# Optimization experiments

Measured on AMD Instinct MI355X. Metric: run time of the kernel, lower is better.

## Reference

```python
import jax, jax.numpy as jnp
import numpy as np
from functools import partial

B, H, W = 2, 480, 480
C, HALF = 32, 16
L, WN, PAD = 4, 20, 20

def gelu(x):
    return jax.nn.gelu(x, approximate=False)

def setup_inputs() -> dict:
    key = jax.random.key(0)
    ks = jax.random.split(key, 24)
    scale = 1.0 / (C * C)
    d = {}
    d["input_data"] = jax.random.normal(ks[0], (B, H, W, 1), jnp.float32)
    d["src_data"] = jax.random.normal(ks[1], (B, H, W, 3), jnp.float32)
    # input lifting MLP: sizes [5, 16, 32]
    d["in_w1"] = jax.random.normal(ks[2], (5, HALF), jnp.float32) * 0.1
    d["in_b1"] = jnp.zeros((HALF,), jnp.float32)
    d["in_w2"] = jax.random.normal(ks[3], (HALF, C), jnp.float32) * 0.1
    d["in_b2"] = jnp.zeros((C,), jnp.float32)
    # eps lifting MLP: sizes [3, 16, 32]
    d["eps_w1"] = jax.random.normal(ks[4], (3, HALF), jnp.float32) * 0.1
    d["eps_b1"] = jnp.zeros((HALF,), jnp.float32)
    d["eps_w2"] = jax.random.normal(ks[5], (HALF, C), jnp.float32) * 0.1
    d["eps_b2"] = jnp.zeros((C,), jnp.float32)
    # Fourier layer params, stacked over L layers
    d["fw1"] = jax.random.uniform(ks[6], (L, C, C, WN, WN, 2), jnp.float32) * scale
    d["fw2"] = jax.random.uniform(ks[7], (L, C, C, WN, WN, 2), jnp.float32) * scale
    d["conv_w"] = jax.random.normal(ks[8], (L, C, C), jnp.float32) * 0.05
    d["conv_b"] = jnp.zeros((L, C), jnp.float32)
    # projection MLP: sizes [32, 16, 2]
    d["proj_w1"] = jax.random.normal(ks[9], (C, HALF), jnp.float32) * 0.1
    d["proj_b1"] = jnp.zeros((HALF,), jnp.float32)
    d["proj_w2"] = jax.random.normal(ks[10], (HALF, 2), jnp.float32) * 0.1
    d["proj_b2"] = jnp.zeros((2,), jnp.float32)
    # mask conv 3x3, 1->1 channel
    d["mask_w"] = jax.random.normal(ks[11], (1, 1, 3, 3), jnp.float32) * 0.1
    d["mask_b"] = jnp.zeros((1,), jnp.float32)
    return d

def _grid(b, h, w):
    gx = jnp.broadcast_to(jnp.linspace(0.0, 1.0, h, dtype=jnp.float32)[None, :, None, None], (b, h, w, 1))
    gy = jnp.broadcast_to(jnp.linspace(0.0, 1.0, w, dtype=jnp.float32)[None, None, :, None], (b, h, w, 1))
    return jnp.concatenate([gx, gy], axis=-1)

def _mlp(x, w1, b1, w2, b2):
    # FCLayer(gelu) then FCLayer(linear)
    return gelu(x @ w1 + b1) @ w2 + b2

def _fourier_conv(x, x_eps, w1, w2):
    # x, x_eps: [B, C, Hp, Wp]
    hp, wp = x.shape[-2], x.shape[-1]
    xf = jnp.fft.rfft2(x * x_eps)                       # [B,C,Hp,Wp//2+1] complex
    xr = jnp.stack([xf.real, xf.imag], axis=-1)         # [B,C,Hp,Wp//2+1,2]
    lo = jnp.einsum('bixyz,ioxyz->boxyz', xr[:, :, :WN, :WN, :], w1)
    hi = jnp.einsum('bixyz,ioxyz->boxyz', xr[:, :, -WN:, :WN, :], w2)
    out = jnp.zeros((x.shape[0], w1.shape[1], hp, wp // 2 + 1, 2), jnp.float32)
    out = out.at[:, :, :WN, :WN, :].set(lo)
    out = out.at[:, :, -WN:, :WN, :].set(hi)
    return jnp.fft.irfft2(out[..., 0] + 1j * out[..., 1], s=(hp, wp))

def _forward(input_data, src_data, in_w1, in_b1, in_w2, in_b2,
             eps_w1, eps_b1, eps_w2, eps_b2, fw1, fw2, conv_w, conv_b,
             proj_w1, proj_b1, proj_w2, proj_b2, mask_w, mask_b):
    b, h, w = input_data.shape[0], input_data.shape[1], input_data.shape[2]
    grid = _grid(b, h, w)
    x_in = jnp.concatenate([src_data, grid], axis=-1)       # [B,H,W,5]
    x_eps = jnp.concatenate([input_data, grid], axis=-1)    # [B,H,W,3]
    field = src_data[..., 1:]                               # [B,H,W,2]

    a = _mlp(x_in, in_w1, in_b1, in_w2, in_b2)              # [B,H,W,C]
    a = jnp.transpose(a, (0, 3, 1, 2))                      # [B,C,H,W]
    a = jnp.pad(a, ((0, 0), (0, 0), (0, PAD), (0, PAD)))    # [B,C,H+P,W+P]
    e = _mlp(x_eps, eps_w1, eps_b1, eps_w2, eps_b2)
    e = jnp.transpose(e, (0, 3, 1, 2))
    e = jnp.pad(e, ((0, 0), (0, 0), (0, PAD), (0, PAD)))

    for l in range(L):
        x1 = _fourier_conv(a, e, fw1[l], fw2[l])
        x2 = jnp.einsum('bihw,oi->bohw', a, conv_w[l]) + conv_b[l][None, :, None, None]
        a = x1 + x2
        if l < L - 1:
            a = gelu(a)

    pred = a[..., :-PAD, :-PAD]                             # [B,C,H,W]
    pred = jnp.transpose(pred, (0, 2, 3, 1))                # [B,H,W,C]
    pred = _mlp(pred, proj_w1, proj_b1, proj_w2, proj_b2)   # [B,H,W,2]

    xm = jnp.transpose(input_data, (0, 3, 1, 2))            # [B,1,H,W]
    mask = jax.lax.conv_general_dilated(xm, mask_w, (1, 1), 'SAME',
                                        dimension_numbers=('NCHW', 'OIHW', 'NCHW'))
    mask = mask + mask_b[None, :, None, None]
    mask = jnp.transpose(mask, (0, 2, 3, 1))                # [B,H,W,1] -> broadcasts over 2
    return field * mask + pred

def reference(input_data, src_data, in_w1, in_b1, in_w2, in_b2,
              eps_w1, eps_b1, eps_w2, eps_b2, fw1, fw2, conv_w, conv_b,
              proj_w1, proj_b1, proj_w2, proj_b2, mask_w, mask_b):
    return _forward(input_data, src_data, in_w1, in_b1, in_w2, in_b2,
                    eps_w1, eps_b1, eps_w2, eps_b2, fw1, fw2, conv_w, conv_b,
                    proj_w1, proj_b1, proj_w2, proj_b2, mask_w, mask_b)
```

## Files before the change

kernel.cpp:

```cpp
#include <hip/hip_runtime.h>
#include <hip/hip_bf16.h>

#define BD 2
#define HD 480
#define WD 480
#define CD 32
#define HALFD 16
#define WND 20
#define NP 500
#define PLANE (HD*WD)
#define TWO_PI_OVER_NP 0.012566370614359172954f

typedef __attribute__((ext_vector_type(8))) short bf16x8;
typedef __attribute__((ext_vector_type(4))) float f32x4;

__device__ __forceinline__ float gelu_f(float x) {
    return 0.5f * x * (1.0f + erff(x * 0.70710678118654752f));
}
__device__ __forceinline__ float bfbits2f(short s) {
    unsigned u = ((unsigned)(unsigned short)s) << 16;
    return __uint_as_float(u);
}
__device__ __forceinline__ short bf16s(float v) {
    __hip_bfloat16 b = __float2bfloat16(v);
    return *reinterpret_cast<short*>(&b);
}
__device__ __forceinline__ unsigned pk2(float a, float b) {
    return (unsigned)(unsigned short)bf16s(a) | ((unsigned)(unsigned short)bf16s(b) << 16);
}
__device__ __forceinline__ unsigned mulpk(unsigned a, unsigned e) {
    return pk2(bfbits2f((short)(a & 0xffff)) * bfbits2f((short)(e & 0xffff)),
               bfbits2f((short)(a >> 16))    * bfbits2f((short)(e >> 16)));
}

__global__ void __launch_bounds__(512) k_aeF1(
    const float* src, const float* inp,
    const float* iw1, const float* ib1,
    const float* iw2, const float* ib2,
    const float* ew1, const float* eb1,
    const float* ew2, const float* eb2,
    const __hip_bfloat16* Twig,
    __hip_bfloat16* A, __hip_bfloat16* E, __hip_bfloat16* Y1)
{
    __shared__ float s_iw1[80], s_ib1[16];
    __shared__ float s_ew1[48], s_eb1[16];
    __shared__ __align__(16) __hip_bfloat16 s_hid[480 * 16];
    __shared__ __align__(16) __hip_bfloat16 sA[32 * 488];

    int tid = threadIdx.x;
    int lane = tid & 63, wv = tid >> 6;
    int c0 = lane & 15, kg = lane >> 4;
    int b = blockIdx.x / HD;
    int h = blockIdx.x % HD;

    if (tid < 80) s_iw1[tid] = iw1[tid];
    if (tid >= 96 && tid < 112) s_ib1[tid - 96] = ib1[tid - 96];
    if (tid >= 128 && tid < 176) s_ew1[tid - 128] = ew1[tid - 128];
    if (tid >= 192 && tid < 208) s_eb1[tid - 192] = eb1[tid - 192];

    bf16x8 bIn[2], bEps[2];
    float biasIn[2], biasEps[2];
    #pragma unroll
    for (int nt = 0; nt < 2; nt++) {
        int c = nt * 16 + c0;
        #pragma unroll
        for (int j = 0; j < 8; j++) {
            int k = kg * 8 + j;
            bIn[nt][j]  = (k < 16) ? bf16s(iw2[k * 32 + c]) : (short)0;
            bEps[nt][j] = (k < 16) ? bf16s(ew2[k * 32 + c]) : (short)0;
        }
        biasIn[nt]  = ib2[c];
        biasEps[nt] = eb2[c];
    }

    float s0 = 0.f, s1 = 0.f, s2 = 0.f, xi = 0.f;
    float gx = (float)h * (1.0f / 479.0f);
    float gy = (float)tid * (1.0f / 479.0f);
    size_t pbase = (size_t)b * PLANE + (size_t)h * WD;
    if (tid < WD) {
        s0 = src[(pbase + tid) * 3 + 0];
        s1 = src[(pbase + tid) * 3 + 1];
        s2 = src[(pbase + tid) * 3 + 2];
        xi = inp[pbase + tid];
    }
    __syncthreads();

    if (tid < WD) {
        unsigned pk[8];
        #pragma unroll
        for (int j = 0; j < 16; j += 2) {
            float v0 = s_ib1[j]     + s0 * s_iw1[j]     + s1 * s_iw1[16 + j]
                     + s2 * s_iw1[32 + j]     + gx * s_iw1[48 + j]     + gy * s_iw1[64 + j];
            float v1 = s_ib1[j + 1] + s0 * s_iw1[j + 1] + s1 * s_iw1[16 + j + 1]
                     + s2 * s_iw1[32 + j + 1] + gx * s_iw1[48 + j + 1] + gy * s_iw1[64 + j + 1];
            pk[j >> 1] = pk2(gelu_f(v0), gelu_f(v1));
        }
        uint4* d = reinterpret_cast<uint4*>(&s_hid[tid * 16]);
        d[0] = make_uint4(pk[0], pk[1], pk[2], pk[3]);
        d[1] = make_uint4(pk[4], pk[5], pk[6], pk[7]);
    }
    __syncthreads();

    for (int t = wv; t < 60; t += 8) {
        int tile = t >> 1, nt = t & 1;
        bf16x8 av = {0, 0, 0, 0, 0, 0, 0, 0};
        if (kg < 2)
            av = *reinterpret_cast<const bf16x8*>(&s_hid[(tile * 16 + c0) * 16 + kg * 8]);
        f32x4 acc = {0.f, 0.f, 0.f, 0.f};
        acc = __builtin_amdgcn_mfma_f32_16x16x32_bf16(av, bIn[nt], acc, 0, 0, 0);
        float bias = biasIn[nt];
        int ch = nt * 16 + c0;
        int px = tile * 16 + kg * 4;
        unsigned w0 = pk2(acc[0] + bias, acc[1] + bias);
        unsigned w1 = pk2(acc[2] + bias, acc[3] + bias);
        *reinterpret_cast<uint2*>(&sA[ch * 488 + px]) = make_uint2(w0, w1);
    }
    __syncthreads();

    {
        __hip_bfloat16* Adst = A + (size_t)b * CD * PLANE + (size_t)h * WD;
        for (int t = tid; t < 32 * 60; t += 512) {
            int row = t / 60, chunk = t % 60;
            uint4 v = *reinterpret_cast<const uint4*>(&sA[row * 488 + chunk * 8]);
            *reinterpret_cast<uint4*>(&Adst[(size_t)row * PLANE + chunk * 8]) = v;
        }
    }
    if (tid < WD) {
        unsigned pk[8];
        #pragma unroll
        for (int j = 0; j < 16; j += 2) {
            float v0 = s_eb1[j]     + xi * s_ew1[j]     + gx * s_ew1[16 + j]     + gy * s_ew1[32 + j];
            float v1 = s_eb1[j + 1] + xi * s_ew1[j + 1] + gx * s_ew1[16 + j + 1] + gy * s_ew1[32 + j + 1];
            pk[j >> 1] = pk2(gelu_f(v0), gelu_f(v1));
        }
        uint4* d = reinterpret_cast<uint4*>(&s_hid[tid * 16]);
        d[0] = make_uint4(pk[0], pk[1], pk[2], pk[3]);
        d[1] = make_uint4(pk[4], pk[5], pk[6], pk[7]);
    }
    __syncthreads();

    for (int t = wv; t < 60; t += 8) {
        int tile = t >> 1, nt = t & 1;
        bf16x8 av = {0, 0, 0, 0, 0, 0, 0, 0};
        if (kg < 2)
            av = *reinterpret_cast<const bf16x8*>(&s_hid[(tile * 16 + c0) * 16 + kg * 8]);
        f32x4 acc = {0.f, 0.f, 0.f, 0.f};
        acc = __builtin_amdgcn_mfma_f32_16x16x32_bf16(av, bEps[nt], acc, 0, 0, 0);
        float bias = biasEps[nt];
        int ch = nt * 16 + c0;
        int px = tile * 16 + kg * 4;
        float e0 = acc[0] + bias, e1 = acc[1] + bias;
        float e2 = acc[2] + bias, e3 = acc[3] + bias;
        *reinterpret_cast<uint2*>(&E[(size_t)(b * 32 + ch) * PLANE + (size_t)h * WD + px])
            = make_uint2(pk2(e0, e1), pk2(e2, e3));
        uint2 a8 = *reinterpret_cast<const uint2*>(&sA[ch * 488 + px]);
        float a0 = bfbits2f((short)(a8.x & 0xffff));
        float a1 = bfbits2f((short)(a8.x >> 16));
        float a2 = bfbits2f((short)(a8.y & 0xffff));
        float a3 = bfbits2f((short)(a8.y >> 16));
        *reinterpret_cast<uint2*>(&sA[ch * 488 + px])
            = make_uint2(pk2(a0 * e0, a1 * e1), pk2(a2 * e2, a3 * e3));
    }
    __syncthreads();

    if (wv < 6) {
        int mt = wv & 1, nt = wv >> 1;
        int c = mt * 16 + c0;
        const __hip_bfloat16* gbase = &sA[c * 488 + (kg << 3)];
        f32x4 a0 = {0.f, 0.f, 0.f, 0.f}, a1 = a0, a2 = a0;
        #pragma unroll
        for (int kt = 0; kt < 15; kt += 3) {
            bf16x8 g0 = *reinterpret_cast<const bf16x8*>(gbase + kt * 32);
            bf16x8 g1 = *reinterpret_cast<const bf16x8*>(gbase + (kt + 1) * 32);
            bf16x8 g2 = *reinterpret_cast<const bf16x8*>(gbase + (kt + 2) * 32);
            bf16x8 b0 = *reinterpret_cast<const bf16x8*>(Twig + (((kt * 3 + nt) << 9) + lane * 8));
            bf16x8 b1 = *reinterpret_cast<const bf16x8*>(Twig + ((((kt + 1) * 3 + nt) << 9) + lane * 8));
            bf16x8 b2 = *reinterpret_cast<const bf16x8*>(Twig + ((((kt + 2) * 3 + nt) << 9) + lane * 8));
            a0 = __builtin_amdgcn_mfma_f32_16x16x32_bf16(g0, b0, a0, 0, 0, 0);
            a1 = __builtin_amdgcn_mfma_f32_16x16x32_bf16(g1, b1, a1, 0, 0, 0);
            a2 = __builtin_amdgcn_mfma_f32_16x16x32_bf16(g2, b2, a2, 0, 0, 0);
        }
        f32x4 acc = a0 + a1 + a2;
        int n = nt * 16 + c0;
        if (n < 40) {
            int ky = n >> 1, part = n & 1;
            int crow = mt * 16 + (kg << 2);
            #pragma unroll
            for (int r = 0; r < 4; r++) {
                int cc = crow + r;
                Y1[((((size_t)(b * 32 + cc)) * WND + ky) * HD + h) * 2 + part] =
                    __float2bfloat16(acc[r]);
            }
        }
    }
}

__global__ void k_tables(__hip_bfloat16* T) {
    int e = blockIdx.x * 256 + threadIdx.x;
    if (e >= 435 * 512) return;
    int tile = e >> 9, r = e & 511;
    int lane = r >> 3, j = r & 7;
    float v = 0.0f;
    if (tile < 45) {
        int kt = tile / 3, nt = tile % 3;
        int k = kt * 32 + ((lane >> 4) << 3) + j;
        int n = nt * 16 + (lane & 15);
        if (n < 40) {
            int ky = n >> 1;
            int idx = (k * ky) % NP;
            float ang = (float)idx * TWO_PI_OVER_NP;
            v = (n & 1) ? -sinf(ang) : cosf(ang);
        }
    } else if (tile < 105) {
        int t2 = tile - 45;
        int nt = t2 >> 1, kt = t2 & 1;
        int kk = kt * 32 + ((lane >> 4) << 3) + j;
        int w = nt * 16 + (lane & 15);
        if (kk < 40) {
            int ky = kk >> 1;
            int idx = (ky * w) % NP;
            float ang = (float)idx * TWO_PI_OVER_NP;
            v = (kk & 1) ? -sinf(ang) : cosf(ang);
        }
    } else if (tile < 255) {
        int t2 = tile - 105;
        int kt = t2 / 5, nt = t2 % 5;
        int k = kt * 32 + ((lane >> 4) << 3) + j;
        int n = nt * 16 + (lane & 15);
        int hh = k >> 1, ri = k & 1;
        int kxi = n >> 1, part = n & 1;
        int kx = (kxi < 20) ? kxi : kxi + 460;
        int idx = (kx * hh) % NP;
        float ang = (float)idx * TWO_PI_OVER_NP;
        float c = cosf(ang), s = sinf(ang);
        v = (part == 0) ? (ri == 0 ? c : s) : (ri == 0 ? -s : c);
    } else {
        int t2 = tile - 255;
        int nt = t2 / 3, kt = t2 % 3;
        int k = kt * 32 + ((lane >> 4) << 3) + j;
        int n = nt * 16 + (lane & 15);
        if (k < 80) {
            int kxi = k >> 1, ri = k & 1;
            int hh = n >> 1, part = n & 1;
            int kx = (kxi < 20) ? kxi : kxi + 460;
            int idx = (kx * hh) % NP;
            float ang = (float)idx * TWO_PI_OVER_NP;
            float c = cosf(ang), s = sinf(ang);
            v = (part == 0) ? (ri == 0 ? c : -s) : (ri == 0 ? s : c);
        }
    }
    T[e] = __float2bfloat16(v);
}

__global__ void __launch_bounds__(64) k_F2m(
    const __hip_bfloat16* Y1, const __hip_bfloat16* Tf2, float* Y2)
{
    int lane = threadIdx.x;
    int task = blockIdx.x;
    int mt = task / 5, nt = task % 5;
    int row = mt * 16 + (lane & 15);
    int koff = (lane >> 4) << 3;
    const __hip_bfloat16* arow = Y1 + (size_t)row * 960 + koff;
    f32x4 a0 = {0.f, 0.f, 0.f, 0.f}, a1 = a0, a2 = a0;
    #pragma unroll
    for (int kt = 0; kt < 30; kt += 3) {
        bf16x8 v0 = *reinterpret_cast<const bf16x8*>(arow + kt * 32);
        bf16x8 v1 = *reinterpret_cast<const bf16x8*>(arow + (kt + 1) * 32);
        bf16x8 v2 = *reinterpret_cast<const bf16x8*>(arow + (kt + 2) * 32);
        bf16x8 b0 = *reinterpret_cast<const bf16x8*>(Tf2 + (((kt * 5 + nt) << 9) + lane * 8));
        bf16x8 b1 = *reinterpret_cast<const bf16x8*>(Tf2 + ((((kt + 1) * 5 + nt) << 9) + lane * 8));
        bf16x8 b2 = *reinterpret_cast<const bf16x8*>(Tf2 + ((((kt + 2) * 5 + nt) << 9) + lane * 8));
        a0 = __builtin_amdgcn_mfma_f32_16x16x32_bf16(v0, b0, a0, 0, 0, 0);
        a1 = __builtin_amdgcn_mfma_f32_16x16x32_bf16(v1, b1, a1, 0, 0, 0);
        a2 = __builtin_amdgcn_mfma_f32_16x16x32_bf16(v2, b2, a2, 0, 0, 0);
    }
    f32x4 acc = a0 + a1 + a2;
    int n = nt * 16 + (lane & 15);
    int mb = mt * 16 + ((lane >> 4) << 2);
    #pragma unroll
    for (int r = 0; r < 4; r++)
        Y2[(size_t)(mb + r) * 80 + n] = acc[r];
}

__global__ void __launch_bounds__(256) k_mix(
    const float* Y2, __hip_bfloat16* Zb,
    const float* fw1, const float* fw2, int l)
{
    int gid = blockIdx.x * 256 + threadIdx.x;
    int col = gid % 96;
    int row = gid / 96;
    if (col >= 80) { Zb[gid] = __float2bfloat16(0.0f); return; }
    int ky = row % 20;
    int oc = (row / 20) % 32;
    int b = row / 640;
    int z = col & 1;
    int kxi = col >> 1;
    const float* wp;
    int x;
    if (kxi < 20) { wp = fw1; x = kxi; } else { wp = fw2; x = kxi - 20; }
    size_t wbase = ((((size_t)(l * 32) * 32 + oc) * 20 + x) * 20 + ky) * 2 + z;
    const float* y2 = Y2 + ((size_t)b * 32 * 20 + ky) * 80 + kxi * 2 + z;
    float acc = 0.f;
    for (int i = 0; i < 32; i++) {
        float yv = y2[(size_t)i * 1600];
        float wv = wp[wbase + (size_t)i * 25600];
        acc += yv * wv;
    }
    Zb[gid] = __float2bfloat16(acc);
}

__global__ void __launch_bounds__(256) k_I1m(
    const __hip_bfloat16* Zb, const __hip_bfloat16* Ti1, __hip_bfloat16* U)
{
    int wv = threadIdx.x >> 6, lane = threadIdx.x & 63;
    int task = blockIdx.x * 4 + wv;
    int mt = task / 60, nt = task % 60;
    int row = mt * 16 + (lane & 15);
    int koff = (lane >> 4) << 3;
    const __hip_bfloat16* arow = Zb + (size_t)row * 96 + koff;
    f32x4 a0 = {0.f, 0.f, 0.f, 0.f}, a1 = a0, a2 = a0;
    {
        bf16x8 v0 = *reinterpret_cast<const bf16x8*>(arow);
        bf16x8 v1 = *reinterpret_cast<const bf16x8*>(arow + 32);
        bf16x8 v2 = *reinterpret_cast<const bf16x8*>(arow + 64);
        bf16x8 b0 = *reinterpret_cast<const bf16x8*>(Ti1 + (((nt * 3 + 0) << 9) + lane * 8));
        bf16x8 b1 = *reinterpret_cast<const bf16x8*>(Ti1 + (((nt * 3 + 1) << 9) + lane * 8));
        bf16x8 b2 = *reinterpret_cast<const bf16x8*>(Ti1 + (((nt * 3 + 2) << 9) + lane * 8));
        a0 = __builtin_amdgcn_mfma_f32_16x16x32_bf16(v0, b0, a0, 0, 0, 0);
        a1 = __builtin_amdgcn_mfma_f32_16x16x32_bf16(v1, b1, a1, 0, 0, 0);
        a2 = __builtin_amdgcn_mfma_f32_16x16x32_bf16(v2, b2, a2, 0, 0, 0);
    }
    f32x4 acc = a0 + a1 + a2;
    int n = nt * 16 + (lane & 15);
    int mb = mt * 16 + ((lane >> 4) << 2);
    #pragma unroll
    for (int r = 0; r < 4; r++)
        U[(size_t)(mb + r) * 960 + n] = __float2bfloat16(acc[r]);
}

__global__ void __launch_bounds__(512) k_I2F1(
    const __hip_bfloat16* U, __hip_bfloat16* A,
    const __hip_bfloat16* E,
    const float* convw, const float* convb,
    const __hip_bfloat16* TinvF, const __hip_bfloat16* Twig,
    __hip_bfloat16* Y1, int l)
{
    __shared__ __align__(16) __hip_bfloat16 sUf[4 * 512];
    __shared__ __align__(16) __hip_bfloat16 sWf[2 * 512];
    __shared__ __align__(16) __hip_bfloat16 sA[32 * 488];
    __shared__ float sB[CD];
    int tid = threadIdx.x;
    int b = blockIdx.x / HD;
    int h = blockIdx.x % HD;
    if (tid < CD) sB[tid] = convb[l * CD + tid];
    for (int t = tid; t < 2048; t += 512) {
        int j = t & 7, lane = (t >> 3) & 63, ktmt = t >> 9;
        int mt = ktmt >> 1, kt = ktmt & 1;
        int oc = mt * 16 + (lane & 15);
        int kk = kt * 32 + ((lane >> 4) << 3) + j;
        float v = 0.f;
        if (kk < 40) {
            int ky = kk >> 1;
            __hip_bfloat162 u = reinterpret_cast<const __hip_bfloat162*>(U)
                [(((size_t)b * CD + oc) * WND + ky) * HD + h];
            float sc = (ky == 0 ? 1.0f : 2.0f) * (1.0f / 250000.0f);
            v = ((kk & 1) ? __bfloat162float(u.y) : __bfloat162float(u.x)) * sc;
        }
        sUf[t] = __float2bfloat16(v);
    }
    for (int t = tid; t < 1024; t += 512) {
        int j = t & 7, lane = (t >> 3) & 63, mt = t >> 9;
        int oc = mt * 16 + (lane & 15);
        int ic = ((lane >> 4) << 3) + j;
        sWf[t] = __float2bfloat16(convw[(size_t)l * CD * CD + oc * CD + ic]);
    }
    __syncthreads();
    int wv = tid >> 6, lane = tid & 63;
    int c0 = lane & 15, kg = lane >> 4;
    const unsigned short* Ap = reinterpret_cast<const unsigned short*>(A)
        + (size_t)b * CD * PLANE + (size_t)h * WD;
    for (int t = wv; t < 60; t += 8) {
        int mt = t & 1, nt = t >> 1;
        bf16x8 bv2;
        #pragma unroll
        for (int j = 0; j < 8; j++)
            bv2[j] = (short)Ap[(size_t)(kg * 8 + j) * PLANE + nt * 16 + c0];
        f32x4 a0 = {0.f, 0.f, 0.f, 0.f}, a1 = a0, a2 = a0;
        bf16x8 u0 = *reinterpret_cast<const bf16x8*>(&sUf[((mt * 2 + 0) << 9) + lane * 8]);
        bf16x8 u1 = *reinterpret_cast<const bf16x8*>(&sUf[((mt * 2 + 1) << 9) + lane * 8]);
        bf16x8 t0 = *reinterpret_cast<const bf16x8*>(TinvF + (((nt * 2 + 0) << 9) + lane * 8));
        bf16x8 t1 = *reinterpret_cast<const bf16x8*>(TinvF + (((nt * 2 + 1) << 9) + lane * 8));
        bf16x8 wf = *reinterpret_cast<const bf16x8*>(&sWf[(mt << 9) + lane * 8]);
        a0 = __builtin_amdgcn_mfma_f32_16x16x32_bf16(u0, t0, a0, 0, 0, 0);
        a1 = __builtin_amdgcn_mfma_f32_16x16x32_bf16(u1, t1, a1, 0, 0, 0);
        a2 = __builtin_amdgcn_mfma_f32_16x16x32_bf16(wf, bv2, a2, 0, 0, 0);
        f32x4 acc = a0 + a1 + a2;
        int w = nt * 16 + c0;
        int ocb = mt * 16 + (kg << 2);
        #pragma unroll
        for (int r = 0; r < 4; r++) {
            short sv = bf16s(gelu_f(acc[r] + sB[ocb + r]));
            sA[(ocb + r) * 488 + w] = *reinterpret_cast<__hip_bfloat16*>(&sv);
        }
    }
    __syncthreads();
    {
        __hip_bfloat16* Adst = A + (size_t)b * CD * PLANE + (size_t)h * WD;
        const __hip_bfloat16* Erow = E + (size_t)b * CD * PLANE + (size_t)h * WD;
        for (int t = tid; t < 32 * 60; t += 512) {
            int row = t / 60, chunk = t % 60;
            uint4 a = *reinterpret_cast<const uint4*>(&sA[row * 488 + chunk * 8]);
            *reinterpret_cast<uint4*>(&Adst[(size_t)row * PLANE + chunk * 8]) = a;
            uint4 e = *reinterpret_cast<const uint4*>(&Erow[(size_t)row * PLANE + chunk * 8]);
            *reinterpret_cast<uint4*>(&sA[row * 488 + chunk * 8]) =
                make_uint4(mulpk(a.x, e.x), mulpk(a.y, e.y),
                           mulpk(a.z, e.z), mulpk(a.w, e.w));
        }
    }
    __syncthreads();
    if (wv < 6) {
        int mt = wv & 1, nt = wv >> 1;
        int c = mt * 16 + c0;
        const __hip_bfloat16* gbase = &sA[c * 488 + (kg << 3)];
        f32x4 a0 = {0.f, 0.f, 0.f, 0.f}, a1 = a0, a2 = a0;
        #pragma unroll
        for (int kt = 0; kt < 15; kt += 3) {
            bf16x8 g0 = *reinterpret_cast<const bf16x8*>(gbase + kt * 32);
            bf16x8 g1 = *reinterpret_cast<const bf16x8*>(gbase + (kt + 1) * 32);
            bf16x8 g2 = *reinterpret_cast<const bf16x8*>(gbase + (kt + 2) * 32);
            bf16x8 b0 = *reinterpret_cast<const bf16x8*>(Twig + (((kt * 3 + nt) << 9) + lane * 8));
            bf16x8 b1 = *reinterpret_cast<const bf16x8*>(Twig + ((((kt + 1) * 3 + nt) << 9) + lane * 8));
            bf16x8 b2 = *reinterpret_cast<const bf16x8*>(Twig + ((((kt + 2) * 3 + nt) << 9) + lane * 8));
            a0 = __builtin_amdgcn_mfma_f32_16x16x32_bf16(g0, b0, a0, 0, 0, 0);
            a1 = __builtin_amdgcn_mfma_f32_16x16x32_bf16(g1, b1, a1, 0, 0, 0);
            a2 = __builtin_amdgcn_mfma_f32_16x16x32_bf16(g2, b2, a2, 0, 0, 0);
        }
        f32x4 acc = a0 + a1 + a2;
        int n = nt * 16 + c0;
        if (n < 40) {
            int ky = n >> 1, part = n & 1;
            int crow = mt * 16 + (kg << 2);
            #pragma unroll
            for (int r = 0; r < 4; r++) {
                int cc = crow + r;
                Y1[((((size_t)(b * 32 + cc)) * WND + ky) * HD + h) * 2 + part] =
                    __float2bfloat16(acc[r]);
            }
        }
    }
}

__global__ void __launch_bounds__(512) k_I2out(
    const __hip_bfloat16* U, const __hip_bfloat16* A,
    const float* convw, const float* convb,
    const __hip_bfloat16* TinvF,
    const float* inp, const float* src,
    const float* pw1, const float* pb1,
    const float* pw2, const float* pb2,
    const float* mw, const float* mb,
    float* out, int l)
{
    __shared__ __align__(16) __hip_bfloat16 sUf[4 * 512];
    __shared__ __align__(16) __hip_bfloat16 sWf[2 * 512];
    __shared__ __align__(16) __hip_bfloat16 sAT[WD * 40];
    __shared__ float sP[WD * 2];
    __shared__ float sB[CD];
    __shared__ float sB1[HALFD], sW2[HALFD * 2], sB2[2], sM[9], sMB[1];
    int tid = threadIdx.x;
    int lane = tid & 63, wv = tid >> 6;
    int c0 = lane & 15, kg = lane >> 4;
    int b = blockIdx.x / HD;
    int h = blockIdx.x % HD;
    if (tid < CD) sB[tid] = convb[l * CD + tid];
    if (tid >= 32 && tid < 48) sB1[tid - 32] = pb1[tid - 32];
    if (tid >= 64 && tid < 96) sW2[tid - 64] = pw2[tid - 64];
    if (tid >= 96 && tid < 98) sB2[tid - 96] = pb2[tid - 96];
    if (tid >= 128 && tid < 137) sM[tid - 128] = mw[tid - 128];
    if (tid == 160) sMB[0] = mb[0];
    bf16x8 bW1;
    #pragma unroll
    for (int j = 0; j < 8; j++)
        bW1[j] = bf16s(pw1[(kg * 8 + j) * 16 + c0]);
    for (int t = tid; t < 2048; t += 512) {
        int j = t & 7, lane2 = (t >> 3) & 63, ktmt = t >> 9;
        int mt = ktmt >> 1, kt = ktmt & 1;
        int oc = mt * 16 + (lane2 & 15);
        int kk = kt * 32 + ((lane2 >> 4) << 3) + j;
        float v = 0.f;
        if (kk < 40) {
            int ky = kk >> 1;
            __hip_bfloat162 u = reinterpret_cast<const __hip_bfloat162*>(U)
                [(((size_t)b * CD + oc) * WND + ky) * HD + h];
            float sc = (ky == 0 ? 1.0f : 2.0f) * (1.0f / 250000.0f);
            v = ((kk & 1) ? __bfloat162float(u.y) : __bfloat162float(u.x)) * sc;
        }
        sUf[t] = __float2bfloat16(v);
    }
    for (int t = tid; t < 1024; t += 512) {
        int j = t & 7, lane2 = (t >> 3) & 63, mt = t >> 9;
        int oc = mt * 16 + (lane2 & 15);
        int ic = ((lane2 >> 4) << 3) + j;
        sWf[t] = __float2bfloat16(convw[(size_t)l * CD * CD + oc * CD + ic]);
    }
    __syncthreads();
    const unsigned short* Ap = reinterpret_cast<const unsigned short*>(A)
        + (size_t)b * CD * PLANE + (size_t)h * WD;
    for (int t = wv; t < 60; t += 8) {
        int mt = t & 1, nt = t >> 1;
        bf16x8 bv2;
        #pragma unroll
        for (int j = 0; j < 8; j++)
            bv2[j] = (short)Ap[(size_t)(kg * 8 + j) * PLANE + nt * 16 + c0];
        f32x4 a0 = {0.f, 0.f, 0.f, 0.f}, a1 = a0, a2 = a0;
        bf16x8 u0 = *reinterpret_cast<const bf16x8*>(&sUf[((mt * 2 + 0) << 9) + lane * 8]);
        bf16x8 u1 = *reinterpret_cast<const bf16x8*>(&sUf[((mt * 2 + 1) << 9) + lane * 8]);
        bf16x8 t0 = *reinterpret_cast<const bf16x8*>(TinvF + (((nt * 2 + 0) << 9) + lane * 8));
        bf16x8 t1 = *reinterpret_cast<const bf16x8*>(TinvF + (((nt * 2 + 1) << 9) + lane * 8));
        bf16x8 wf = *reinterpret_cast<const bf16x8*>(&sWf[(mt << 9) + lane * 8]);
        a0 = __builtin_amdgcn_mfma_f32_16x16x32_bf16(u0, t0, a0, 0, 0, 0);
        a1 = __builtin_amdgcn_mfma_f32_16x16x32_bf16(u1, t1, a1, 0, 0, 0);
        a2 = __builtin_amdgcn_mfma_f32_16x16x32_bf16(wf, bv2, a2, 0, 0, 0);
        f32x4 acc = a0 + a1 + a2;
        int w = nt * 16 + c0;
        int ocb = mt * 16 + (kg << 2);
        unsigned q0 = pk2(acc[0] + sB[ocb + 0], acc[1] + sB[ocb + 1]);
        unsigned q1 = pk2(acc[2] + sB[ocb + 2], acc[3] + sB[ocb + 3]);
        *reinterpret_cast<uint2*>(&sAT[w * 40 + ocb]) = make_uint2(q0, q1);
    }
    __syncthreads();
    for (int t = wv; t < 30; t += 8) {
        bf16x8 av = *reinterpret_cast<const bf16x8*>(&sAT[(t * 16 + c0) * 40 + kg * 8]);
        f32x4 acc = {0.f, 0.f, 0.f, 0.f};
        acc = __builtin_amdgcn_mfma_f32_16x16x32_bf16(av, bW1, acc, 0, 0, 0);
        #pragma unroll
        for (int r = 0; r < 4; r++) {
            float hid = gelu_f(acc[r] + sB1[c0]);
            float p0 = hid * sW2[c0 * 2 + 0];
            float p1 = hid * sW2[c0 * 2 + 1];
            #pragma unroll
            for (int m = 1; m < 16; m <<= 1) {
                p0 += __shfl_xor(p0, m, 64);
                p1 += __shfl_xor(p1, m, 64);
            }
            if (c0 == 0) {
                int px = t * 16 + kg * 4 + r;
                sP[px * 2 + 0] = p0 + sB2[0];
                sP[px * 2 + 1] = p1 + sB2[1];
            }
        }
    }
    __syncthreads();
    for (int w = tid; w < WD; w += 512) {
        float p0 = sP[w * 2 + 0];
        float p1 = sP[w * 2 + 1];
        float m = sMB[0];
        #pragma unroll
        for (int dh = 0; dh < 3; dh++) {
            int hh = h + dh - 1;
            #pragma unroll
            for (int dw = 0; dw < 3; dw++) {
                int ww = w + dw - 1;
                if (hh >= 0 && hh < HD && ww >= 0 && ww < WD)
                    m += inp[(size_t)b * PLANE + (size_t)hh * WD + ww] * sM[dh * 3 + dw];
            }
        }
        size_t gid = (size_t)b * PLANE + (size_t)h * WD + w;
        float f0 = src[gid * 3 + 1];
        float f1 = src[gid * 3 + 2];
        out[gid * 2 + 0] = f0 * m + p0;
        out[gid * 2 + 1] = f1 * m + p1;
    }
}

extern "C" void kernel_launch(void* const* d_in, const int* in_sizes, int n_in,
                              void* d_out, int out_size, void* d_ws, size_t ws_size,
                              hipStream_t stream) {
    const float* inp = (const float*)d_in[0];
    const float* src = (const float*)d_in[1];
    const float* iw1 = (const float*)d_in[2];
    const float* ib1 = (const float*)d_in[3];
    const float* iw2 = (const float*)d_in[4];
    const float* ib2 = (const float*)d_in[5];
    const float* ew1 = (const float*)d_in[6];
    const float* eb1 = (const float*)d_in[7];
    const float* ew2 = (const float*)d_in[8];
    const float* eb2 = (const float*)d_in[9];
    const float* fw1 = (const float*)d_in[10];
    const float* fw2 = (const float*)d_in[11];
    const float* cw  = (const float*)d_in[12];
    const float* cb  = (const float*)d_in[13];
    const float* pw1 = (const float*)d_in[14];
    const float* pb1 = (const float*)d_in[15];
    const float* pw2 = (const float*)d_in[16];
    const float* pb2 = (const float*)d_in[17];
    const float* mw  = (const float*)d_in[18];
    const float* mb  = (const float*)d_in[19];

    const size_t NA = (size_t)BD * CD * PLANE;
    __hip_bfloat16* A   = (__hip_bfloat16*)d_ws;
    __hip_bfloat16* E   = A + NA;
    __hip_bfloat16* Y1U = E + NA;
    float* Y2 = (float*)(Y1U + (size_t)BD * CD * WND * HD * 2);
    __hip_bfloat16* Zb = (__hip_bfloat16*)(Y2 + 1280 * 80);
    __hip_bfloat16* Tbl   = Zb + 1280 * 96;
    __hip_bfloat16* Twig  = Tbl;
    __hip_bfloat16* TinvF = Twig + 45 * 512;
    __hip_bfloat16* Tf2   = TinvF + 60 * 512;
    __hip_bfloat16* Ti1   = Tf2 + 150 * 512;

    k_tables<<<870, 256, 0, stream>>>(Tbl);
    k_aeF1<<<BD * HD, 512, 0, stream>>>(src, inp, iw1, ib1, iw2, ib2,
                                        ew1, eb1, ew2, eb2, Twig, A, E, Y1U);
    for (int l = 0; l < 4; l++) {
        k_F2m<<<400, 64, 0, stream>>>(Y1U, Tf2, Y2);
        k_mix<<<480, 256, 0, stream>>>(Y2, Zb, fw1, fw2, l);
        k_I1m<<<1200, 256, 0, stream>>>(Zb, Ti1, Y1U);
        if (l < 3)
            k_I2F1<<<BD * HD, 512, 0, stream>>>(Y1U, A, E, cw, cb, TinvF, Twig,
                                                Y1U, l);
        else
            k_I2out<<<BD * HD, 512, 0, stream>>>(Y1U, A, cw, cb, TinvF,
                                                 inp, src, pw1, pb1, pw2, pb2,
                                                 mw, mb, (float*)d_out, l);
    }
}
```

Before: 350.2 us.

## Fuse first inverse-DFT stage into I2 kernels, computing twiddles per row

Removes the separate k_I1m MFMA kernel and its U intermediate. Each I2F1/I2out block now computes the per-row inverse DFT along the first axis itself from Zb, using on-the-fly cos/sin twiddles in shared memory, and writes the result straight into the MFMA-layout shared buffer. This saves one launch per layer and the global write and reread of U. In exchange every block redoes a 640x40 complex dot product in scalar FP32 and reads all of Zb for its batch, which lengthens each block's prologue.

```diff
diff --git a/kernel.cpp b/kernel.cpp
--- a/kernel.cpp
+++ b/kernel.cpp
@@ -309,37 +309,8 @@
     Zb[gid] = __float2bfloat16(acc);
 }
 
-__global__ void __launch_bounds__(256) k_I1m(
-    const __hip_bfloat16* Zb, const __hip_bfloat16* Ti1, __hip_bfloat16* U)
-{
-    int wv = threadIdx.x >> 6, lane = threadIdx.x & 63;
-    int task = blockIdx.x * 4 + wv;
-    int mt = task / 60, nt = task % 60;
-    int row = mt * 16 + (lane & 15);
-    int koff = (lane >> 4) << 3;
-    const __hip_bfloat16* arow = Zb + (size_t)row * 96 + koff;
-    f32x4 a0 = {0.f, 0.f, 0.f, 0.f}, a1 = a0, a2 = a0;
-    {
-        bf16x8 v0 = *reinterpret_cast<const bf16x8*>(arow);
-        bf16x8 v1 = *reinterpret_cast<const bf16x8*>(arow + 32);
-        bf16x8 v2 = *reinterpret_cast<const bf16x8*>(arow + 64);
-        bf16x8 b0 = *reinterpret_cast<const bf16x8*>(Ti1 + (((nt * 3 + 0) << 9) + lane * 8));
-        bf16x8 b1 = *reinterpret_cast<const bf16x8*>(Ti1 + (((nt * 3 + 1) << 9) + lane * 8));
-        bf16x8 b2 = *reinterpret_cast<const bf16x8*>(Ti1 + (((nt * 3 + 2) << 9) + lane * 8));
-        a0 = __builtin_amdgcn_mfma_f32_16x16x32_bf16(v0, b0, a0, 0, 0, 0);
-        a1 = __builtin_amdgcn_mfma_f32_16x16x32_bf16(v1, b1, a1, 0, 0, 0);
-        a2 = __builtin_amdgcn_mfma_f32_16x16x32_bf16(v2, b2, a2, 0, 0, 0);
-    }
-    f32x4 acc = a0 + a1 + a2;
-    int n = nt * 16 + (lane & 15);
-    int mb = mt * 16 + ((lane >> 4) << 2);
-    #pragma unroll
-    for (int r = 0; r < 4; r++)
-        U[(size_t)(mb + r) * 960 + n] = __float2bfloat16(acc[r]);
-}
-
 __global__ void __launch_bounds__(512) k_I2F1(
-    const __hip_bfloat16* U, __hip_bfloat16* A,
+    const __hip_bfloat16* Zb, __hip_bfloat16* A,
     const __hip_bfloat16* E,
     const float* convw, const float* convb,
     const __hip_bfloat16* TinvF, const __hip_bfloat16* Twig,
@@ -349,30 +320,54 @@
     __shared__ __align__(16) __hip_bfloat16 sWf[2 * 512];
     __shared__ __align__(16) __hip_bfloat16 sA[32 * 488];
     __shared__ float sB[CD];
+    __shared__ float2 sCS[40];
     int tid = threadIdx.x;
     int b = blockIdx.x / HD;
     int h = blockIdx.x % HD;
     if (tid < CD) sB[tid] = convb[l * CD + tid];
+    if (tid >= 64 && tid < 104) {
+        int kxi = tid - 64;
+        int kx = (kxi < 20) ? kxi : kxi + 460;
+        int idx = (kx * h) % NP;
+        float ang = (float)idx * TWO_PI_OVER_NP;
+        sCS[kxi] = make_float2(cosf(ang), sinf(ang));
+    }
     for (int t = tid; t < 2048; t += 512) {
-        int j = t & 7, lane = (t >> 3) & 63, ktmt = t >> 9;
-        int mt = ktmt >> 1, kt = ktmt & 1;
-        int oc = mt * 16 + (lane & 15);
-        int kk = kt * 32 + ((lane >> 4) << 3) + j;
-        float v = 0.f;
-        if (kk < 40) {
-            int ky = kk >> 1;
-            __hip_bfloat162 u = reinterpret_cast<const __hip_bfloat162*>(U)
-                [(((size_t)b * CD + oc) * WND + ky) * HD + h];
-            float sc = (ky == 0 ? 1.0f : 2.0f) * (1.0f / 250000.0f);
-            v = ((kk & 1) ? __bfloat162float(u.y) : __bfloat162float(u.x)) * sc;
-        }
-        sUf[t] = __float2bfloat16(v);
+        int j = t & 7, lane2 = (t >> 3) & 63, kt = (t >> 9) & 1;
+        int kk = kt * 32 + ((lane2 >> 4) << 3) + j;
+        if (kk >= 40) sUf[t] = __float2bfloat16(0.0f);
     }
     for (int t = tid; t < 1024; t += 512) {
-        int j = t & 7, lane = (t >> 3) & 63, mt = t >> 9;
-        int oc = mt * 16 + (lane & 15);
-        int ic = ((lane >> 4) << 3) + j;
+        int j = t & 7, lane2 = (t >> 3) & 63, mt = t >> 9;
+        int oc = mt * 16 + (lane2 & 15);
+        int ic = ((lane2 >> 4) << 3) + j;
         sWf[t] = __float2bfloat16(convw[(size_t)l * CD * CD + oc * CD + ic]);
+    }
+    __syncthreads();
+    for (int p = tid; p < 640; p += 512) {
+        int oc = p / 20, ky = p % 20;
+        const uint4* zrow = reinterpret_cast<const uint4*>(Zb + (size_t)(b * 640 + p) * 96);
+        float acc0 = 0.f, acc1 = 0.f;
+        #pragma unroll
+        for (int q = 0; q < 10; q++) {
+            uint4 z = zrow[q];
+            unsigned zz[4] = {z.x, z.y, z.z, z.w};
+            #pragma unroll
+            for (int e2 = 0; e2 < 4; e2++) {
+                float Zr = bfbits2f((short)(zz[e2] & 0xffff));
+                float Zi = bfbits2f((short)(zz[e2] >> 16));
+                float2 cs = sCS[q * 4 + e2];
+                acc0 += Zr * cs.x - Zi * cs.y;
+                acc1 += Zr * cs.y + Zi * cs.x;
+            }
+        }
+        float sc = (ky == 0 ? 1.0f : 2.0f) * (1.0f / 250000.0f);
+        int mtc = oc >> 4, c = oc & 15;
+        int kk0 = 2 * ky, kk1 = 2 * ky + 1;
+        int t0 = ((mtc * 2 + (kk0 >> 5)) << 9) | (((((kk0 & 31) >> 3) << 4) | c) << 3) | (kk0 & 7);
+        int t1 = ((mtc * 2 + (kk1 >> 5)) << 9) | (((((kk1 & 31) >> 3) << 4) | c) << 3) | (kk1 & 7);
+        sUf[t0] = __float2bfloat16(acc0 * sc);
+        sUf[t1] = __float2bfloat16(acc1 * sc);
     }
     __syncthreads();
     int wv = tid >> 6, lane = tid & 63;
@@ -451,7 +446,7 @@
 }
 
 __global__ void __launch_bounds__(512) k_I2out(
-    const __hip_bfloat16* U, const __hip_bfloat16* A,
+    const __hip_bfloat16* Zb, const __hip_bfloat16* A,
     const float* convw, const float* convb,
     const __hip_bfloat16* TinvF,
     const float* inp, const float* src,
@@ -466,6 +461,7 @@
     __shared__ float sP[WD * 2];
     __shared__ float sB[CD];
     __shared__ float sB1[HALFD], sW2[HALFD * 2], sB2[2], sM[9], sMB[1];
+    __shared__ float2 sCS[40];
     int tid = threadIdx.x;
     int lane = tid & 63, wv = tid >> 6;
     int c0 = lane & 15, kg = lane >> 4;
@@ -473,34 +469,57 @@
     int h = blockIdx.x % HD;
     if (tid < CD) sB[tid] = convb[l * CD + tid];
     if (tid >= 32 && tid < 48) sB1[tid - 32] = pb1[tid - 32];
-    if (tid >= 64 && tid < 96) sW2[tid - 64] = pw2[tid - 64];
-    if (tid >= 96 && tid < 98) sB2[tid - 96] = pb2[tid - 96];
-    if (tid >= 128 && tid < 137) sM[tid - 128] = mw[tid - 128];
-    if (tid == 160) sMB[0] = mb[0];
+    if (tid >= 160 && tid < 192) sW2[tid - 160] = pw2[tid - 160];
+    if (tid >= 192 && tid < 194) sB2[tid - 192] = pb2[tid - 192];
+    if (tid >= 208 && tid < 217) sM[tid - 208] = mw[tid - 208];
+    if (tid == 224) sMB[0] = mb[0];
+    if (tid >= 64 && tid < 104) {
+        int kxi = tid - 64;
+        int kx = (kxi < 20) ? kxi : kxi + 460;
+        int idx = (kx * h) % NP;
+        float ang = (float)idx * TWO_PI_OVER_NP;
+        sCS[kxi] = make_float2(cosf(ang), sinf(ang));
+    }
     bf16x8 bW1;
     #pragma unroll
     for (int j = 0; j < 8; j++)
         bW1[j] = bf16s(pw1[(kg * 8 + j) * 16 + c0]);
     for (int t = tid; t < 2048; t += 512) {
-        int j = t & 7, lane2 = (t >> 3) & 63, ktmt = t >> 9;
-        int mt = ktmt >> 1, kt = ktmt & 1;
-        int oc = mt * 16 + (lane2 & 15);
+        int j = t & 7, lane2 = (t >> 3) & 63, kt = (t >> 9) & 1;
         int kk = kt * 32 + ((lane2 >> 4) << 3) + j;
-        float v = 0.f;
-        if (kk < 40) {
-            int ky = kk >> 1;
-            __hip_bfloat162 u = reinterpret_cast<const __hip_bfloat162*>(U)
-                [(((size_t)b * CD + oc) * WND + ky) * HD + h];
-            float sc = (ky == 0 ? 1.0f : 2.0f) * (1.0f / 250000.0f);
-            v = ((kk & 1) ? __bfloat162float(u.y) : __bfloat162float(u.x)) * sc;
-        }
-        sUf[t] = __float2bfloat16(v);
+        if (kk >= 40) sUf[t] = __float2bfloat16(0.0f);
     }
     for (int t = tid; t < 1024; t += 512) {
         int j = t & 7, lane2 = (t >> 3) & 63, mt = t >> 9;
         int oc = mt * 16 + (lane2 & 15);
         int ic = ((lane2 >> 4) << 3) + j;
         sWf[t] = __float2bfloat16(convw[(size_t)l * CD * CD + oc * CD + ic]);
+    }
+    __syncthreads();
+    for (int p = tid; p < 640; p += 512) {
+        int oc = p / 20, ky = p % 20;
+        const uint4* zrow = reinterpret_cast<const uint4*>(Zb + (size_t)(b * 640 + p) * 96);
+        float acc0 = 0.f, acc1 = 0.f;
+        #pragma unroll
+        for (int q = 0; q < 10; q++) {
+            uint4 z = zrow[q];
+            unsigned zz[4] = {z.x, z.y, z.z, z.w};
+            #pragma unroll
+            for (int e2 = 0; e2 < 4; e2++) {
+                float Zr = bfbits2f((short)(zz[e2] & 0xffff));
+                float Zi = bfbits2f((short)(zz[e2] >> 16));
+                float2 cs = sCS[q * 4 + e2];
+                acc0 += Zr * cs.x - Zi * cs.y;
+                acc1 += Zr * cs.y + Zi * cs.x;
+            }
+        }
+        float sc = (ky == 0 ? 1.0f : 2.0f) * (1.0f / 250000.0f);
+        int mtc = oc >> 4, c = oc & 15;
+        int kk0 = 2 * ky, kk1 = 2 * ky + 1;
+        int t0 = ((mtc * 2 + (kk0 >> 5)) << 9) | (((((kk0 & 31) >> 3) << 4) | c) << 3) | (kk0 & 7);
+        int t1 = ((mtc * 2 + (kk1 >> 5)) << 9) | (((((kk1 & 31) >> 3) << 4) | c) << 3) | (kk1 & 7);
+        sUf[t0] = __float2bfloat16(acc0 * sc);
+        sUf[t1] = __float2bfloat16(acc1 * sc);
     }
     __syncthreads();
     const unsigned short* Ap = reinterpret_cast<const unsigned short*>(A)
@@ -606,7 +625,6 @@
     __hip_bfloat16* Twig  = Tbl;
     __hip_bfloat16* TinvF = Twig + 45 * 512;
     __hip_bfloat16* Tf2   = TinvF + 60 * 512;
-    __hip_bfloat16* Ti1   = Tf2 + 150 * 512;
 
     k_tables<<<870, 256, 0, stream>>>(Tbl);
     k_aeF1<<<BD * HD, 512, 0, stream>>>(src, inp, iw1, ib1, iw2, ib2,
@@ -614,12 +632,11 @@
     for (int l = 0; l < 4; l++) {
         k_F2m<<<400, 64, 0, stream>>>(Y1U, Tf2, Y2);
         k_mix<<<480, 256, 0, stream>>>(Y2, Zb, fw1, fw2, l);
-        k_I1m<<<1200, 256, 0, stream>>>(Zb, Ti1, Y1U);
         if (l < 3)
-            k_I2F1<<<BD * HD, 512, 0, stream>>>(Y1U, A, E, cw, cb, TinvF, Twig,
+            k_I2F1<<<BD * HD, 512, 0, stream>>>(Zb, A, E, cw, cb, TinvF, Twig,
                                                 Y1U, l);
         else
-            k_I2out<<<BD * HD, 512, 0, stream>>>(Y1U, A, cw, cb, TinvF,
+            k_I2out<<<BD * HD, 512, 0, stream>>>(Zb, A, cw, cb, TinvF,
                                                  inp, src, pw1, pb1, pw2, pb2,
                                                  mw, mb, (float*)d_out, l);
     }
```

Measured after the change: 641.2 us. 83.1% more time.
